# Optimization experiments

Hardware: AMD Instinct MI355X
Metric: run time of the kernel (lower is better)

## Reference

```python
import jax, jax.numpy as jnp
import numpy as np
import math

D_MODEL = 2048
N_HEADS = 16
D_FF = 8192
SEQ = 2048
BATCH = 2
THETA = 10000.0
EPS = 1e-5


def _rope(x, pos):
    # x: [B, H, S, d_k] ; pos: [B, S] int
    d = x.shape[-1]
    inv_freq = 1.0 / (THETA ** (jnp.arange(0, d, 2, dtype=jnp.float32) / d))  # [d/2]
    ang = pos[..., None].astype(jnp.float32) * inv_freq  # [B, S, d/2]
    cos = jnp.cos(ang)[:, None, :, :, None]  # [B,1,S,d/2,1]
    sin = jnp.sin(ang)[:, None, :, :, None]
    xr = x.reshape(*x.shape[:-1], d // 2, 2)
    x1, x2 = xr[..., 0], xr[..., 1]
    rot = jnp.stack((-x2, x1), axis=-1)  # rotate pairs
    out = xr * cos + rot * sin
    return out.reshape(x.shape)


def _trunc_normal(key, shape, in_f, out_f):
    std = math.sqrt(2.0 / (in_f + out_f))
    return jax.random.truncated_normal(key, -3.0, 3.0, shape, jnp.float32) * std


def setup_inputs() -> dict:
    key = jax.random.key(0)
    ks = jax.random.split(key, 8)
    x = jax.random.normal(ks[0], (BATCH, SEQ, D_MODEL), jnp.float32)
    token_positions = jnp.sort(jax.random.randint(ks[1], (BATCH, SEQ), 0, SEQ), axis=-1)
    W_qkv = _trunc_normal(ks[2], (3 * D_MODEL, D_MODEL), D_MODEL, 3 * D_MODEL)
    W_o = _trunc_normal(ks[3], (D_MODEL, D_MODEL), D_MODEL, D_MODEL)
    W1 = _trunc_normal(ks[4], (D_FF, D_MODEL), D_MODEL, D_FF)
    W3 = _trunc_normal(ks[5], (D_FF, D_MODEL), D_MODEL, D_FF)
    W2 = _trunc_normal(ks[6], (D_MODEL, D_FF), D_FF, D_MODEL)
    g1 = jnp.ones((D_MODEL,), jnp.float32)
    g2 = jnp.ones((D_MODEL,), jnp.float32)
    return {"x": x, "token_positions": token_positions, "W_qkv": W_qkv, "W_o": W_o,
            "g1": g1, "g2": g2, "W1": W1, "W3": W3, "W2": W2}


def _rmsnorm(x, g):
    xf = x.astype(jnp.float32)
    rms = jnp.sqrt(jnp.mean(xf * xf, axis=-1, keepdims=True) + EPS)
    return (xf / rms * g).astype(x.dtype)


def reference(x, token_positions, W_qkv, W_o, g1, g2, W1, W3, W2):
    B, S, D = x.shape
    H = N_HEADS
    dk = D // H
    # --- attention sublayer ---
    h = _rmsnorm(x, g1)
    qkv = jnp.einsum('bsi,oi->bso', h, W_qkv)  # [B,S,3D]
    q, k, v = jnp.split(qkv, 3, axis=-1)
    to_heads = lambda t: t.reshape(B, S, H, dk).transpose(0, 2, 1, 3)  # [B,H,S,dk]
    q, k, v = to_heads(q), to_heads(k), to_heads(v)
    q = _rope(q, token_positions)
    k = _rope(k, token_positions)
    scores = jnp.einsum('bhnd,bhmd->bhnm', q, k) / math.sqrt(dk)  # [B,H,S,S]
    mask = jnp.tril(jnp.ones((S, S), dtype=bool))
    scores = jnp.where(mask, scores, -jnp.inf)
    attn = jax.nn.softmax(scores, axis=-1)
    o = jnp.einsum('bhnm,bhmd->bhnd', attn, v)
    o = o.transpose(0, 2, 1, 3).reshape(B, S, D)
    x = x + jnp.einsum('bsi,oi->bso', o, W_o)
    # --- SwiGLU FFN sublayer ---
    h2 = _rmsnorm(x, g2)
    x1 = jnp.einsum('bsi,oi->bso', h2, W1)
    x3 = jnp.einsum('bsi,oi->bso', h2, W3)
    x = x + jnp.einsum('bsi,oi->bso', jax.nn.silu(x1) * x3, W2)
    return x
```

## Files before the change

### kernel.cpp

```cpp
#include <hip/hip_runtime.h>

#define DEV __device__ __forceinline__

typedef __bf16 bf16x8 __attribute__((ext_vector_type(8)));
typedef float f32x4 __attribute__((ext_vector_type(4)));
typedef unsigned short u16x8 __attribute__((ext_vector_type(8)));
typedef unsigned short u16x2 __attribute__((ext_vector_type(2)));

DEV unsigned short f2bf(float f) {
  unsigned int u = __float_as_uint(f);
  u += 0x7fffu + ((u >> 16) & 1u);
  return (unsigned short)(u >> 16);
}
DEV float bf2f(unsigned short h) {
  return __uint_as_float(((unsigned int)h) << 16);
}
DEV void gload16(const void* g, void* l) {
  __builtin_amdgcn_global_load_lds(
      (const __attribute__((address_space(1))) unsigned int*)g,
      (__attribute__((address_space(3))) unsigned int*)l, 16, 0, 0);
}
DEV f32x4 mfma16(bf16x8 a, bf16x8 b, f32x4 c) {
  return __builtin_amdgcn_mfma_f32_16x16x32_bf16(a, b, c, 0, 0, 0);
}

#define SB   __builtin_amdgcn_s_barrier()
#define SCH  __builtin_amdgcn_sched_barrier(0)
#define LGKM0 asm volatile("s_waitcnt lgkmcnt(0)" ::: "memory")
#define PRIO1 __builtin_amdgcn_s_setprio(1)
#define PRIO0 __builtin_amdgcn_s_setprio(0)

__global__ __launch_bounds__(256) void k_cvt(const float* __restrict__ in,
                                             unsigned short* __restrict__ out, int n8) {
  const int stride = gridDim.x * 256;
  for (int i = blockIdx.x * 256 + threadIdx.x; i < n8; i += stride) {
    const float4* p = (const float4*)(in + (long)i * 8);
    const float4 a = p[0], b = p[1];
    u16x8 o = { f2bf(a.x), f2bf(a.y), f2bf(a.z), f2bf(a.w),
                f2bf(b.x), f2bf(b.y), f2bf(b.z), f2bf(b.w) };
    *(u16x8*)(out + (long)i * 8) = o;
  }
}

__global__ __launch_bounds__(256) void k_add(float* __restrict__ out,
                                             const float* __restrict__ p, int n4) {
  const int stride = gridDim.x * 256;
  for (int i = blockIdx.x * 256 + threadIdx.x; i < n4; i += stride) {
    float4 a = ((const float4*)out)[i];
    const float4 b = ((const float4*)p)[i];
    a.x += b.x; a.y += b.y; a.z += b.z; a.w += b.w;
    ((float4*)out)[i] = a;
  }
}

__global__ __launch_bounds__(256) void k_rmsnorm(const float* __restrict__ x,
                                                 const float* __restrict__ g,
                                                 unsigned short* __restrict__ out) {
  const int row = blockIdx.x;
  const int t = threadIdx.x;
  const float4* xr = (const float4*)(x + (long)row * 2048);
  const float4 a = xr[t * 2], c = xr[t * 2 + 1];
  float ss = a.x * a.x + a.y * a.y + a.z * a.z + a.w * a.w +
             c.x * c.x + c.y * c.y + c.z * c.z + c.w * c.w;
#pragma unroll
  for (int o = 32; o > 0; o >>= 1) ss += __shfl_down(ss, o);
  __shared__ float ws4[4];
  __shared__ float invs;
  if ((t & 63) == 0) ws4[t >> 6] = ss;
  __syncthreads();
  if (t == 0) invs = 1.0f / sqrtf((ws4[0] + ws4[1] + ws4[2] + ws4[3]) * (1.0f / 2048.0f) + 1e-5f);
  __syncthreads();
  const float inv = invs;
  const float4* gr = (const float4*)g;
  const float4 g0 = gr[t * 2], g1v = gr[t * 2 + 1];
  u16x8 o8 = { f2bf(a.x * inv * g0.x),  f2bf(a.y * inv * g0.y),
               f2bf(a.z * inv * g0.z),  f2bf(a.w * inv * g0.w),
               f2bf(c.x * inv * g1v.x), f2bf(c.y * inv * g1v.y),
               f2bf(c.z * inv * g1v.z), f2bf(c.w * inv * g1v.w) };
  *(u16x8*)(out + (long)row * 2048 + t * 8) = o8;
}

template <int EPI>
__global__ __launch_bounds__(512, 2) void k_gemm256(
    const unsigned short* __restrict__ A, const unsigned short* __restrict__ B,
    unsigned short* __restrict__ outBF, float* __restrict__ outF,
    const float* __restrict__ resid, const unsigned short* __restrict__ aux,
    float* __restrict__ partial, int M, int N, int K, int Keff) {
  __shared__ __align__(16) unsigned short lds[2][2][2][128][64];
  const int tid = threadIdx.x;
  const int wid = tid >> 6, lane = tid & 63;
  const int wr = wid >> 2, wc = wid & 3;
  const int fr = lane & 15, g4 = lane >> 4;

  const int nwg = gridDim.x;
  int bid = blockIdx.x;
  { int q = nwg >> 3, r = nwg & 7, xcd = bid & 7, lo = bid >> 3;
    bid = (xcd < r ? xcd * (q + 1) : r * (q + 1) + (xcd - r) * q) + lo; }
  int tile = bid, ks = 0;
  if constexpr (EPI == 3) { ks = bid & 1; tile = bid >> 1; }
  const int nxb = N >> 8;
  const int bx = tile % nxb, by = tile / nxb;
  const int arow0 = by << 8, bcol0 = bx << 8;
  const int NT = Keff >> 6;

  const int srow = tid >> 3;
  const int sg = (tid & 7) ^ (srow & 7);
  const unsigned short* Asrc = A + (long)(arow0 + srow) * K + (long)ks * Keff + (sg << 3);
  const unsigned short* Bsrc = B + (long)(bcol0 + srow) * K + (long)ks * Keff + (sg << 3);

  const int posk0 = (g4 ^ (lane & 7)) << 3;
  const int posk1 = ((4 + g4) ^ (lane & 7)) << 3;

  f32x4 acc[8][4] = {};
  bf16x8 a[4][2], b0[2][2], b1[2][2];

#define VM6  asm volatile("s_waitcnt vmcnt(6)" ::: "memory")
#define STAGE(SRC, xs, bufi, mat, h)                                            \
  { const unsigned short* s_ = (SRC) + (long)(h) * 128 * K + (long)(xs) * 64;   \
    unsigned short* d_ = &lds[bufi][mat][h][0][0] + wid * 512;                  \
    gload16(s_, d_);                                                            \
    gload16(s_ + (long)64 * K, d_ + 4096); }
#define RD_A(mh)                                                                \
  _Pragma("unroll") for (int m_ = 0; m_ < 4; ++m_) {                            \
    const unsigned short* p_ = baseA + ((mh) * 64 + m_ * 16 + fr) * 64;         \
    a[m_][0] = *(const bf16x8*)(p_ + posk0);                                    \
    a[m_][1] = *(const bf16x8*)(p_ + posk1); }
#define RD_B(arr, nh)                                                           \
  _Pragma("unroll") for (int n_ = 0; n_ < 2; ++n_) {                            \
    const unsigned short* p_ = baseB + ((nh) * 32 + n_ * 16 + fr) * 64;         \
    arr[n_][0] = *(const bf16x8*)(p_ + posk0);                                  \
    arr[n_][1] = *(const bf16x8*)(p_ + posk1); }
#define MM(mh, nh, Bv)                                                          \
  _Pragma("unroll") for (int k_ = 0; k_ < 2; ++k_)                              \
  _Pragma("unroll") for (int m_ = 0; m_ < 4; ++m_)                              \
  _Pragma("unroll") for (int n_ = 0; n_ < 2; ++n_)                              \
    acc[(mh)*4+m_][(nh)*2+n_] = mfma16(a[m_][k_], Bv[n_][k_], acc[(mh)*4+m_][(nh)*2+n_]);

  STAGE(Asrc, 0, 0, 0, 0);
  STAGE(Asrc, 0, 0, 0, 1);
  STAGE(Bsrc, 0, 0, 1, 0);
  STAGE(Bsrc, 0, 0, 1, 1);
  { const int x1p = (NT > 1) ? 1 : 0;
    STAGE(Bsrc, x1p, 1, 1, 0);
    STAGE(Bsrc, x1p, 1, 1, 1);
    STAGE(Asrc, x1p, 1, 0, 0); }
  VM6; SCH; SB; SCH;

  for (int t = 0; t < NT; ++t) {
    const unsigned short* baseA = &lds[t & 1][0][wr][0][0];
    const unsigned short* baseB = &lds[t & 1][1][wc >> 1][0][0] + (wc & 1) * 4096;
    const int x1 = (t + 1 < NT) ? t + 1 : NT - 1;
    const int x2 = (t + 2 < NT) ? t + 2 : NT - 1;
    const int bn = (t + 1) & 1, bc = t & 1;

    RD_A(0); RD_B(b0, 0);
    STAGE(Asrc, x1, bn, 0, 1);
    SCH; SB; LGKM0; SCH;
    PRIO1; MM(0, 0, b0); PRIO0;
    SCH; SB; SCH;

    RD_B(b1, 1);
    SCH; SB; LGKM0; SCH;
    PRIO1; MM(0, 1, b1); PRIO0;
    SCH; SB; SCH;

    RD_A(1);
    STAGE(Bsrc, x2, bc, 1, 0);
    SCH; SB; LGKM0; SCH;
    PRIO1; MM(1, 1, b1); PRIO0;
    SCH; SB; SCH;

    STAGE(Asrc, x2, bc, 0, 0);
    STAGE(Bsrc, x2, bc, 1, 1);
    SCH;
    PRIO1; MM(1, 0, b0); PRIO0;
    VM6;
    SCH; SB; SCH;
  }
#undef VM6
#undef STAGE
#undef RD_A
#undef RD_B
#undef MM

  const int er = g4 << 2;
#pragma unroll
  for (int m = 0; m < 8; ++m) {
#pragma unroll
    for (int n = 0; n < 4; ++n) {
      const int grow = arow0 + wr * 128 + m * 16 + er;
      const int gcol = bcol0 + wc * 64 + n * 16 + fr;
#pragma unroll
      for (int r = 0; r < 4; ++r) {
        const long idx = (long)(grow + r) * N + gcol;
        const float v = acc[m][n][r];
        if constexpr (EPI == 0) {
          outBF[idx] = f2bf(v);
        } else if constexpr (EPI == 1) {
          outF[idx] = resid[idx] + v;
        } else if constexpr (EPI == 2) {
          const float x1v = bf2f(aux[idx]);
          const float sl = x1v / (1.0f + __expf(-x1v));
          outBF[idx] = f2bf(sl * v);
        } else {
          if (ks == 0) outF[idx] = resid[idx] + v;
          else         partial[idx] = v;
        }
      }
    }
  }
}

__global__ __launch_bounds__(512, 1) void k_gemm_n128(
    const unsigned short* __restrict__ A, const unsigned short* __restrict__ B,
    float* __restrict__ outF, const float* __restrict__ resid, int M, int N, int K) {
  __shared__ __align__(16) unsigned short lds[3][384 * 64];
  const int tid = threadIdx.x;
  const int wid = tid >> 6, lane = tid & 63;
  const int wr = wid >> 1, wc = wid & 1;
  const int fr = lane & 15, g4 = lane >> 4;

  const int nwg = gridDim.x;
  int bid = blockIdx.x;
  { int q = nwg >> 3, r = nwg & 7, xcd = bid & 7, lo = bid >> 3;
    bid = (xcd < r ? xcd * (q + 1) : r * (q + 1) + (xcd - r) * q) + lo; }
  const int nxb = N >> 7;
  const int bx = bid % nxb, by = bid / nxb;
  const int arow0 = by << 8, bcol0 = bx << 7;
  const int NT = K >> 6;

  const int srow = tid >> 3;
  const int sg = (tid & 7) ^ (srow & 7);
  const unsigned short* Asrc = A + (long)(arow0 + srow) * K + (sg << 3);
  const unsigned short* Bsrc = B + (long)(bcol0 + srow) * K + (sg << 3);

  const int posk0 = (g4 ^ (lane & 7)) << 3;
  const int posk1 = ((4 + g4) ^ (lane & 7)) << 3;

  f32x4 acc[4][4] = {};
  bf16x8 a[4][2], bl[2][2], bh[2][2];

#define VM6 asm volatile("s_waitcnt vmcnt(6)" ::: "memory")
#define SITE_A(xs, bufi, s)                                                    \
  gload16(Asrc + (long)((s) * 64) * K + (long)(xs) * 64,                       \
          &lds[bufi][(s) * 4096] + wid * 512);
#define SITE_B(xs, bufi, s)                                                    \
  gload16(Bsrc + (long)((s) * 64) * K + (long)(xs) * 64,                       \
          &lds[bufi][16384 + (s) * 4096] + wid * 512);
#define RDA                                                                    \
  _Pragma("unroll") for (int m_ = 0; m_ < 4; ++m_) {                           \
    const unsigned short* p_ = bufb + (wr * 64 + m_ * 16 + fr) * 64;           \
    a[m_][0] = *(const bf16x8*)(p_ + posk0);                                   \
    a[m_][1] = *(const bf16x8*)(p_ + posk1); }
#define RDB(arr, off)                                                          \
  _Pragma("unroll") for (int n_ = 0; n_ < 2; ++n_) {                           \
    const unsigned short* p_ = bufb + 16384 + (wc * 64 + (off) + n_ * 16 + fr) * 64; \
    arr[n_][0] = *(const bf16x8*)(p_ + posk0);                                 \
    arr[n_][1] = *(const bf16x8*)(p_ + posk1); }
#define MMN(nh, Bv)                                                            \
  _Pragma("unroll") for (int k_ = 0; k_ < 2; ++k_)                             \
  _Pragma("unroll") for (int m_ = 0; m_ < 4; ++m_)                             \
  _Pragma("unroll") for (int n_ = 0; n_ < 2; ++n_)                             \
    acc[m_][(nh)*2+n_] = mfma16(a[m_][k_], Bv[n_][k_], acc[m_][(nh)*2+n_]);

  SITE_A(0, 0, 0); SITE_A(0, 0, 1); SITE_A(0, 0, 2); SITE_A(0, 0, 3);
  SITE_B(0, 0, 0); SITE_B(0, 0, 1);
  { const int x1p = (NT > 1) ? 1 : 0;
    SITE_A(x1p, 1, 0); SITE_A(x1p, 1, 1); SITE_A(x1p, 1, 2); SITE_A(x1p, 1, 3);
    SITE_B(x1p, 1, 0); SITE_B(x1p, 1, 1); }
  VM6; SCH; SB; SCH;

  for (int t = 0; t < NT; ++t) {
    const unsigned short* bufb = lds[t % 3];
    const int bn = (t + 2) % 3;
    const int xs = (t + 2 < NT) ? t + 2 : NT - 1;

    RDA; RDB(bl, 0);
    SITE_A(xs, bn, 0); SITE_A(xs, bn, 1);
    SCH; SB; LGKM0; SCH;
    PRIO1; MMN(0, bl); PRIO0;
    SCH; SB; SCH;

    RDB(bh, 32);
    SITE_A(xs, bn, 2); SITE_A(xs, bn, 3); SITE_B(xs, bn, 0); SITE_B(xs, bn, 1);
    SCH; SB; LGKM0; SCH;
    PRIO1; MMN(1, bh); PRIO0;
    VM6;
    SCH; SB; SCH;
  }
#undef VM6
#undef SITE_A
#undef SITE_B
#undef RDA
#undef RDB
#undef MMN

  const int er = g4 << 2;
#pragma unroll
  for (int m = 0; m < 4; ++m) {
#pragma unroll
    for (int n = 0; n < 4; ++n) {
      const int grow = arow0 + wr * 64 + m * 16 + er;
      const int gcol = bcol0 + wc * 64 + n * 16 + fr;
#pragma unroll
      for (int r = 0; r < 4; ++r) {
        const long idx = (long)(grow + r) * N + gcol;
        outF[idx] = resid[idx] + acc[m][n][r];
      }
    }
  }
}

__global__ __launch_bounds__(256) void k_rope(const unsigned short* __restrict__ qkv,
                                              const int* __restrict__ tp,
                                              unsigned short* __restrict__ Qh,
                                              unsigned short* __restrict__ Kh, int S) {
  const int row = blockIdx.x;
  const int b = row / S, s = row - b * S;
  const float pos = (float)tp[row];
  for (int p = threadIdx.x; p < 1024; p += 256) {
    const int h = p >> 6, j = p & 63;
    const float ang = pos * __expf((float)j * -0.14391156831212787f);
    const float cc = cosf(ang), sn = sinf(ang);
    const long ib = (long)row * 6144 + h * 128 + (j << 1);
    const float q1 = bf2f(qkv[ib]), q2 = bf2f(qkv[ib + 1]);
    const float k1 = bf2f(qkv[ib + 2048]), k2v = bf2f(qkv[ib + 2049]);
    const long ob = (((long)(b * 16 + h)) * S + s) * 128 + (j << 1);
    u16x2 qo = { f2bf(q1 * cc - q2 * sn), f2bf(q2 * cc + q1 * sn) };
    u16x2 ko = { f2bf(k1 * cc - k2v * sn), f2bf(k2v * cc + k1 * sn) };
    *(u16x2*)&Qh[ob] = qo;
    *(u16x2*)&Kh[ob] = ko;
  }
}

__global__ __launch_bounds__(256) void k_vtrans(const unsigned short* __restrict__ qkv,
                                                unsigned short* __restrict__ Vt, int S) {
  __shared__ __align__(16) unsigned short t[128 * 72];
  const int bh = blockIdx.x, b = bh >> 4, h = bh & 15;
  const int s0 = blockIdx.y << 6;
  const int tid = threadIdx.x;
#pragma unroll
  for (int it = 0; it < 4; ++it) {
    const int sl = it * 16 + (tid >> 4);
    const int c = tid & 15;
    u16x8 v = *(const u16x8*)(qkv + ((long)(b * S + s0 + sl)) * 6144 + 4096 + h * 128 + (c << 3));
#pragma unroll
    for (int jj = 0; jj < 8; ++jj) t[(c * 8 + jj) * 72 + sl] = v[jj];
  }
  __syncthreads();
  const int d = tid >> 1, half = tid & 1;
  unsigned short* dst = Vt + ((long)bh * 128 + d) * S + s0 + half * 32;
  const unsigned short* srcr = &t[d * 72 + half * 32];
#pragma unroll
  for (int u = 0; u < 4; ++u)
    *(u16x8*)(dst + u * 8) = *(const u16x8*)(srcr + u * 8);
}

__global__ __launch_bounds__(256) void k_attn(const unsigned short* __restrict__ Q,
                                              const unsigned short* __restrict__ Kh,
                                              const unsigned short* __restrict__ Vt,
                                              unsigned short* __restrict__ O, int S) {
  __shared__ __align__(16) unsigned short lds_k[64 * 128];
  __shared__ __align__(16) unsigned short lds_v[128 * 64];
  __shared__ __align__(16) unsigned short lds_p[4 * 16 * 64];
  const int bh = blockIdx.x;
  const int b = bh >> 4, h = bh & 15;
  const int qt = gridDim.y - 1 - blockIdx.y;
  const int q0 = qt << 6;
  const int tid = threadIdx.x, w = tid >> 6, lane = tid & 63;
  const int fr = lane & 15, g4 = lane >> 4;

  bf16x8 qf[4];
  {
    const unsigned short* qb = Q + ((long)bh * S + q0 + w * 16 + fr) * 128 + (g4 << 3);
#pragma unroll
    for (int kk = 0; kk < 4; ++kk) qf[kk] = *(const bf16x8*)(qb + kk * 32);
  }

  f32x4 accO[8] = {};
  float mrow[4], lrow[4];
#pragma unroll
  for (int r = 0; r < 4; ++r) { mrow[r] = -1e30f; lrow[r] = 0.f; }

  const int k_row = (w << 4) + g4;
  const int k_cb = fr << 4;
  const int v_row = (w << 5) + (lane >> 3);
  const int v_cb = (lane & 7) << 4;
  const long kbase = (long)bh * S * 128;
  const long vbase = (long)bh * 128 * S;

  const int ntile = qt + 1;
  for (int it = 0; it < ntile; ++it) {
    const int kv0 = it << 6;
#pragma unroll
    for (int j = 0; j < 4; ++j) {
      const int kr = k_row + j * 4;
      const int kc = k_cb ^ ((kr & 7) << 4);
      gload16(Kh + kbase + (long)(kv0 + kr) * 128 + (kc >> 1), &lds_k[w * 2048 + j * 512]);
      const int vr = v_row + j * 8;
      const int vc = v_cb ^ ((vr & 7) << 4);
      gload16(Vt + vbase + (long)vr * S + kv0 + (vc >> 1), &lds_v[w * 2048 + j * 512]);
    }
    __syncthreads();

    f32x4 sc[4] = {};
#pragma unroll
    for (int kk = 0; kk < 4; ++kk) {
      const int kb = (kk << 6) + (g4 << 4);
#pragma unroll
      for (int n = 0; n < 4; ++n) {
        const int krw = n * 16 + fr;
        const int swz = (krw & 7) << 4;
        bf16x8 kf = *(const bf16x8*)&lds_k[krw * 128 + ((kb ^ swz) >> 1)];
        sc[n] = mfma16(qf[kk], kf, sc[n]);
      }
    }

    const float scl = 0.08838834764831845f;
    float sv[4][4];
    const bool needmask = (kv0 + 63 > q0 + w * 16);
#pragma unroll
    for (int n = 0; n < 4; ++n)
#pragma unroll
      for (int r = 0; r < 4; ++r) {
        float v = sc[n][r] * scl;
        if (needmask) {
          const int qi = q0 + w * 16 + (g4 << 2) + r;
          const int ki = kv0 + n * 16 + fr;
          if (ki > qi) v = -1e30f;
        }
        sv[n][r] = v;
      }
    float corr[4];
#pragma unroll
    for (int r = 0; r < 4; ++r) {
      float tm = fmaxf(fmaxf(sv[0][r], sv[1][r]), fmaxf(sv[2][r], sv[3][r]));
      tm = fmaxf(tm, __shfl_xor(tm, 1));
      tm = fmaxf(tm, __shfl_xor(tm, 2));
      tm = fmaxf(tm, __shfl_xor(tm, 4));
      tm = fmaxf(tm, __shfl_xor(tm, 8));
      const float mn = fmaxf(mrow[r], tm);
      corr[r] = __expf(mrow[r] - mn);
      mrow[r] = mn;
    }
    float rs[4] = {0.f, 0.f, 0.f, 0.f};
#pragma unroll
    for (int n = 0; n < 4; ++n)
#pragma unroll
      for (int r = 0; r < 4; ++r) {
        const float p = __expf(sv[n][r] - mrow[r]);
        rs[r] += p;
        const int pr = (g4 << 2) + r;
        const int pc = (n * 16 + fr) << 1;
        lds_p[(w << 10) + pr * 64 + ((pc ^ ((pr & 7) << 4)) >> 1)] = f2bf(p);
      }
#pragma unroll
    for (int r = 0; r < 4; ++r) {
      float s = rs[r];
      s += __shfl_xor(s, 1);
      s += __shfl_xor(s, 2);
      s += __shfl_xor(s, 4);
      s += __shfl_xor(s, 8);
      lrow[r] = lrow[r] * corr[r] + s;
    }
#pragma unroll
    for (int cb = 0; cb < 8; ++cb)
#pragma unroll
      for (int r = 0; r < 4; ++r) accO[cb][r] *= corr[r];

#pragma unroll
    for (int kk = 0; kk < 2; ++kk) {
      const int pb = (kk << 6) + (g4 << 4);
      bf16x8 pf = *(const bf16x8*)&lds_p[(w << 10) + fr * 64 + ((pb ^ ((fr & 7) << 4)) >> 1)];
#pragma unroll
      for (int cb = 0; cb < 8; ++cb) {
        const int vrw = cb * 16 + fr;
        bf16x8 vf = *(const bf16x8*)&lds_v[vrw * 64 + ((pb ^ ((vrw & 7) << 4)) >> 1)];
        accO[cb] = mfma16(pf, vf, accO[cb]);
      }
    }
    __syncthreads();
  }

#pragma unroll
  for (int cb = 0; cb < 8; ++cb)
#pragma unroll
    for (int r = 0; r < 4; ++r) {
      const int si = q0 + w * 16 + (g4 << 2) + r;
      const float o = accO[cb][r] / lrow[r];
      O[((long)b * S + si) * 2048 + h * 128 + cb * 16 + fr] = f2bf(o);
    }
}

extern "C" void kernel_launch(void* const* d_in, const int* in_sizes, int n_in,
                              void* d_out, int out_size, void* d_ws, size_t ws_size,
                              hipStream_t stream) {
  const float* x    = (const float*)d_in[0];
  const int*   tp   = (const int*)d_in[1];
  const float* Wqkv = (const float*)d_in[2];
  const float* Wo   = (const float*)d_in[3];
  const float* g1   = (const float*)d_in[4];
  const float* g2   = (const float*)d_in[5];
  const float* W1   = (const float*)d_in[6];
  const float* W3   = (const float*)d_in[7];
  const float* W2   = (const float*)d_in[8];
  float* out = (float*)d_out;

  char* ws = (char*)d_ws;
  const size_t MB = 1024 * 1024;
  unsigned short* Qh      = (unsigned short*)(ws + 0 * MB);
  unsigned short* Kh      = (unsigned short*)(ws + 16 * MB);
  unsigned short* Vt      = (unsigned short*)(ws + 32 * MB);
  unsigned short* O_bf    = (unsigned short*)(ws + 48 * MB);
  unsigned short* t_bf    = (unsigned short*)(ws + 0 * MB);
  unsigned short* qkv_bf  = (unsigned short*)(ws + 64 * MB);
  float*          x2      = (float*)         (ws + 64 * MB);
  unsigned short* h2_bf   = (unsigned short*)(ws + 96 * MB);
  unsigned short* wo_bf   = (unsigned short*)(ws + 96 * MB);
  unsigned short* wqkv_bf = (unsigned short*)(ws + 112 * MB);
  unsigned short* w1_bf   = (unsigned short*)(ws + 112 * MB);
  unsigned short* w2_bf   = (unsigned short*)(ws + 112 * MB);
  unsigned short* h1_bf   = (unsigned short*)(ws + 144 * MB);
  unsigned short* w3_bf   = (unsigned short*)(ws + 144 * MB);
  float*          part    = (float*)         (ws + 144 * MB);

  const int S = 2048;

  k_cvt<<<1024, 256, 0, stream>>>(Wqkv, wqkv_bf, 12582912 / 8);
  k_rmsnorm<<<4096, 256, 0, stream>>>(x, g1, h1_bf);
  k_gemm256<0><<<dim3(384), 512, 0, stream>>>(h1_bf, wqkv_bf, qkv_bf, nullptr, nullptr, nullptr, nullptr, 4096, 6144, 2048, 2048);
  k_rope<<<4096, 256, 0, stream>>>(qkv_bf, tp, Qh, Kh, S);
  k_vtrans<<<dim3(32, 32), 256, 0, stream>>>(qkv_bf, Vt, S);
  k_cvt<<<1024, 256, 0, stream>>>(Wo, wo_bf, 4194304 / 8);
  k_cvt<<<1024, 256, 0, stream>>>(W1, w1_bf, 16777216 / 8);
  k_cvt<<<1024, 256, 0, stream>>>(W3, w3_bf, 16777216 / 8);
  k_attn<<<dim3(32, 32), 256, 0, stream>>>(Qh, Kh, Vt, O_bf, S);
  k_gemm_n128<<<dim3(256), 512, 0, stream>>>(O_bf, wo_bf, x2, x, 4096, 2048, 2048);

  k_rmsnorm<<<4096, 256, 0, stream>>>(x2, g2, h2_bf);
  k_gemm256<0><<<dim3(512), 512, 0, stream>>>(h2_bf, w1_bf, t_bf, nullptr, nullptr, nullptr, nullptr, 4096, 8192, 2048, 2048);
  k_cvt<<<1024, 256, 0, stream>>>(W2, w2_bf, 16777216 / 8);
  k_gemm256<2><<<dim3(512), 512, 0, stream>>>(h2_bf, w3_bf, t_bf, nullptr, nullptr, t_bf, nullptr, 4096, 8192, 2048, 2048);
  k_gemm256<3><<<dim3(256), 512, 0, stream>>>(t_bf, w2_bf, nullptr, out, x2, nullptr, part, 4096, 2048, 8192, 4096);
  k_add<<<2048, 256, 0, stream>>>(out, part, 2097152);
}
```

Before: 756.6 us.

## Prefetch next tile's LDS fragments and relax barriers in both GEMM main loops

Both GEMM kernels now read the first A/B register fragments of the next k-tile at the end of each iteration. The first MFMA group then waits only on partial LDS completion (lgkmcnt(4)) and no longer on a full drain, and the loops run with fewer block-wide barriers. The goal is to hide LDS read latency behind MFMA work and cut synchronisation stalls. The cost is more live registers and reordered LDS hazards, where correctness depends on the remaining barriers and vmcnt waits.

```diff
diff --git a/kernel.cpp b/kernel.cpp
--- a/kernel.cpp
+++ b/kernel.cpp
@@ -27,6 +27,8 @@
 #define SB   __builtin_amdgcn_s_barrier()
 #define SCH  __builtin_amdgcn_sched_barrier(0)
 #define LGKM0 asm volatile("s_waitcnt lgkmcnt(0)" ::: "memory")
+#define LGKM4 asm volatile("s_waitcnt lgkmcnt(4)" ::: "memory")
+#define VM6  asm volatile("s_waitcnt vmcnt(6)" ::: "memory")
 #define PRIO1 __builtin_amdgcn_s_setprio(1)
 #define PRIO0 __builtin_amdgcn_s_setprio(0)
 
@@ -114,20 +116,19 @@
   f32x4 acc[8][4] = {};
   bf16x8 a[4][2], b0[2][2], b1[2][2];
 
-#define VM6  asm volatile("s_waitcnt vmcnt(6)" ::: "memory")
 #define STAGE(SRC, xs, bufi, mat, h)                                            \
   { const unsigned short* s_ = (SRC) + (long)(h) * 128 * K + (long)(xs) * 64;   \
     unsigned short* d_ = &lds[bufi][mat][h][0][0] + wid * 512;                  \
     gload16(s_, d_);                                                            \
     gload16(s_ + (long)64 * K, d_ + 4096); }
-#define RD_A(mh)                                                                \
+#define RD_A(BA, mh)                                                            \
   _Pragma("unroll") for (int m_ = 0; m_ < 4; ++m_) {                            \
-    const unsigned short* p_ = baseA + ((mh) * 64 + m_ * 16 + fr) * 64;         \
+    const unsigned short* p_ = (BA) + ((mh) * 64 + m_ * 16 + fr) * 64;          \
     a[m_][0] = *(const bf16x8*)(p_ + posk0);                                    \
     a[m_][1] = *(const bf16x8*)(p_ + posk1); }
-#define RD_B(arr, nh)                                                           \
+#define RD_B(BB, arr, nh)                                                       \
   _Pragma("unroll") for (int n_ = 0; n_ < 2; ++n_) {                            \
-    const unsigned short* p_ = baseB + ((nh) * 32 + n_ * 16 + fr) * 64;         \
+    const unsigned short* p_ = (BB) + ((nh) * 32 + n_ * 16 + fr) * 64;          \
     arr[n_][0] = *(const bf16x8*)(p_ + posk0);                                  \
     arr[n_][1] = *(const bf16x8*)(p_ + posk1); }
 #define MM(mh, nh, Bv)                                                          \
@@ -145,39 +146,43 @@
     STAGE(Bsrc, x1p, 1, 1, 1);
     STAGE(Asrc, x1p, 1, 0, 0); }
   VM6; SCH; SB; SCH;
+  {
+    const unsigned short* baseA = &lds[0][0][wr][0][0];
+    const unsigned short* baseB = &lds[0][1][wc >> 1][0][0] + (wc & 1) * 4096;
+    RD_A(baseA, 0); RD_B(baseB, b0, 0);
+  }
 
   for (int t = 0; t < NT; ++t) {
     const unsigned short* baseA = &lds[t & 1][0][wr][0][0];
     const unsigned short* baseB = &lds[t & 1][1][wc >> 1][0][0] + (wc & 1) * 4096;
+    const unsigned short* baseA2 = &lds[(t + 1) & 1][0][wr][0][0];
+    const unsigned short* baseB2 = &lds[(t + 1) & 1][1][wc >> 1][0][0] + (wc & 1) * 4096;
     const int x1 = (t + 1 < NT) ? t + 1 : NT - 1;
     const int x2 = (t + 2 < NT) ? t + 2 : NT - 1;
     const int bn = (t + 1) & 1, bc = t & 1;
 
-    RD_A(0); RD_B(b0, 0);
+    SB;
+    RD_B(baseB, b1, 1);
     STAGE(Asrc, x1, bn, 0, 1);
-    SCH; SB; LGKM0; SCH;
+    LGKM4; SCH;
     PRIO1; MM(0, 0, b0); PRIO0;
-    SCH; SB; SCH;
-
-    RD_B(b1, 1);
-    SCH; SB; LGKM0; SCH;
+    LGKM0; SCH;
     PRIO1; MM(0, 1, b1); PRIO0;
-    SCH; SB; SCH;
-
-    RD_A(1);
+
+    SB;
+    RD_A(baseA, 1);
     STAGE(Bsrc, x2, bc, 1, 0);
-    SCH; SB; LGKM0; SCH;
+    LGKM0; SCH;
     PRIO1; MM(1, 1, b1); PRIO0;
-    SCH; SB; SCH;
-
+
+    SB;
     STAGE(Asrc, x2, bc, 0, 0);
     STAGE(Bsrc, x2, bc, 1, 1);
-    SCH;
     PRIO1; MM(1, 0, b0); PRIO0;
-    VM6;
-    SCH; SB; SCH;
-  }
-#undef VM6
+    VM6; SCH; SB; SCH;
+    RD_A(baseA2, 0);
+    RD_B(baseB2, b0, 0);
+  }
 #undef STAGE
 #undef RD_A
 #undef RD_B
@@ -240,21 +245,20 @@
   f32x4 acc[4][4] = {};
   bf16x8 a[4][2], bl[2][2], bh[2][2];
 
-#define VM6 asm volatile("s_waitcnt vmcnt(6)" ::: "memory")
 #define SITE_A(xs, bufi, s)                                                    \
   gload16(Asrc + (long)((s) * 64) * K + (long)(xs) * 64,                       \
           &lds[bufi][(s) * 4096] + wid * 512);
 #define SITE_B(xs, bufi, s)                                                    \
   gload16(Bsrc + (long)((s) * 64) * K + (long)(xs) * 64,                       \
           &lds[bufi][16384 + (s) * 4096] + wid * 512);
-#define RDA                                                                    \
+#define RDA(BUF)                                                               \
   _Pragma("unroll") for (int m_ = 0; m_ < 4; ++m_) {                           \
-    const unsigned short* p_ = bufb + (wr * 64 + m_ * 16 + fr) * 64;           \
+    const unsigned short* p_ = (BUF) + (wr * 64 + m_ * 16 + fr) * 64;          \
     a[m_][0] = *(const bf16x8*)(p_ + posk0);                                   \
     a[m_][1] = *(const bf16x8*)(p_ + posk1); }
-#define RDB(arr, off)                                                          \
+#define RDB(BUF, arr, off)                                                     \
   _Pragma("unroll") for (int n_ = 0; n_ < 2; ++n_) {                           \
-    const unsigned short* p_ = bufb + 16384 + (wc * 64 + (off) + n_ * 16 + fr) * 64; \
+    const unsigned short* p_ = (BUF) + 16384 + (wc * 64 + (off) + n_ * 16 + fr) * 64; \
     arr[n_][0] = *(const bf16x8*)(p_ + posk0);                                 \
     arr[n_][1] = *(const bf16x8*)(p_ + posk1); }
 #define MMN(nh, Bv)                                                            \
@@ -269,26 +273,25 @@
     SITE_A(x1p, 1, 0); SITE_A(x1p, 1, 1); SITE_A(x1p, 1, 2); SITE_A(x1p, 1, 3);
     SITE_B(x1p, 1, 0); SITE_B(x1p, 1, 1); }
   VM6; SCH; SB; SCH;
+  RDA(lds[0]); RDB(lds[0], bl, 0);
 
   for (int t = 0; t < NT; ++t) {
     const unsigned short* bufb = lds[t % 3];
+    const unsigned short* bufn = lds[(t + 1) % 3];
     const int bn = (t + 2) % 3;
     const int xs = (t + 2 < NT) ? t + 2 : NT - 1;
 
-    RDA; RDB(bl, 0);
+    SB;
+    RDB(bufb, bh, 32);
     SITE_A(xs, bn, 0); SITE_A(xs, bn, 1);
-    SCH; SB; LGKM0; SCH;
+    LGKM4; SCH;
     PRIO1; MMN(0, bl); PRIO0;
-    SCH; SB; SCH;
-
-    RDB(bh, 32);
     SITE_A(xs, bn, 2); SITE_A(xs, bn, 3); SITE_B(xs, bn, 0); SITE_B(xs, bn, 1);
-    SCH; SB; LGKM0; SCH;
+    LGKM0; SCH;
     PRIO1; MMN(1, bh); PRIO0;
-    VM6;
-    SCH; SB; SCH;
-  }
-#undef VM6
+    VM6; SCH; SB; SCH;
+    RDA(bufn); RDB(bufn, bl, 0);
+  }
 #undef SITE_A
 #undef SITE_B
 #undef RDA
```

Result: no change. 752.0 us (-0.6%).
